# Kernel tuning notes

Measured on AMD Instinct MI355X. Metric: run time of the kernel, lower is better.

## Reference

```python
import jax, jax.numpy as jnp
import numpy as np
import math

B, N, D, H = 4, 2048, 1024, 16
DH = D // H  # dim per head
OUT = 1024

def setup_inputs() -> dict:
    key0 = jax.random.key(0)
    ks = jax.random.split(key0, 12)
    s = 1.0 / math.sqrt(D)
    return {
        "key": jax.random.normal(ks[0], (B, N, D), jnp.float32),
        "value": jax.random.normal(ks[1], (B, N, D), jnp.float32),
        "query": jax.random.normal(ks[2], (B, N, D), jnp.float32),
        "Wk": jax.random.normal(ks[3], (D, D), jnp.float32) * s,
        "bk": jax.random.normal(ks[4], (D,), jnp.float32) * 0.01,
        "Wv": jax.random.normal(ks[5], (D, D), jnp.float32) * s,
        "bv": jax.random.normal(ks[6], (D,), jnp.float32) * 0.01,
        "Wq": jax.random.normal(ks[7], (D, D), jnp.float32) * s,
        "bq": jax.random.normal(ks[8], (D,), jnp.float32) * 0.01,
        "Wo": jax.random.normal(ks[9], (D, OUT), jnp.float32) * s,
        "bo": jax.random.normal(ks[10], (OUT,), jnp.float32) * 0.01,
    }

def reference(key, value, query, Wk, bk, Wv, bv, Wq, bq, Wo, bo):
    scale = math.sqrt(DH)
    k = (key @ Wk + bk).reshape(B, N, H, DH).transpose(0, 2, 1, 3)    # [B,H,N,DH]
    v = (value @ Wv + bv).reshape(B, N, H, DH).transpose(0, 2, 1, 3)
    q = ((query @ Wq + bq) / scale).reshape(B, N, H, DH).transpose(0, 2, 1, 3)
    scores = jnp.einsum('bhqd,bhkd->bhqk', q, k).astype(jnp.float32)  # [B,H,N,N]
    attn = jax.nn.softmax(scores, axis=-1).astype(q.dtype)
    # dropout p=0.0 (eval / identity)
    ctx = jnp.einsum('bhqk,bhkd->bhqd', attn, v)                      # [B,H,N,DH]
    ctx = ctx.transpose(0, 2, 1, 3).reshape(B, N, D)
    out = ctx @ Wo + bo                                               # [B,N,OUT]
    return out
```

## Files before the change

### kernel.cpp

```cpp
#include <hip/hip_runtime.h>
#include <hip/hip_bf16.h>
#include <stdint.h>

#define BB 4
#define NN 2048
#define DD 1024
#define HH 16
#define DHH 64
#define MM (BB*NN)

typedef unsigned short u16;
typedef unsigned int u32;
typedef __bf16 bf16x8_t __attribute__((ext_vector_type(8)));
typedef float f32x4_t __attribute__((ext_vector_type(4)));
typedef float f32x16_t __attribute__((ext_vector_type(16)));

__device__ inline u16 f2b(float f) {
    __hip_bfloat16 h = __float2bfloat16(f);
    return *(u16*)&h;
}

__device__ inline u32 pack2(float lo, float hi) {
    __hip_bfloat162 h2 = __float22bfloat162_rn(make_float2(lo, hi));
    return *(u32*)&h2;
}

__device__ inline void gload16(const void* g, void* l) {
    __builtin_amdgcn_global_load_lds(
        (const __attribute__((address_space(1))) void*)g,
        (__attribute__((address_space(3))) void*)l, 16, 0, 0);
}

__global__ void cvt_kernel(const float* __restrict__ in, u16* __restrict__ out) {
    int i = (blockIdx.x * 256 + threadIdx.x) * 4;
    float4 v = *(const float4*)(in + i);
    ushort4 o;
    o.x = f2b(v.x); o.y = f2b(v.y); o.z = f2b(v.z); o.w = f2b(v.w);
    *(ushort4*)(out + i) = o;
}

__global__ void wtrans_kernel(const float* __restrict__ W0, const float* __restrict__ W1,
                              const float* __restrict__ W2, const float* __restrict__ W3,
                              u16* __restrict__ out_base) {
    int z = blockIdx.z;
    const float* W = (z == 0) ? W0 : (z == 1) ? W1 : (z == 2) ? W2 : W3;
    u16* o = out_base + (size_t)z * DD * DD;
    __shared__ float tile[64][65];
    int t = threadIdx.x;
    int r0 = t >> 6;
    int c = t & 63;
    int kb = blockIdx.x, nb = blockIdx.y;
#pragma unroll
    for (int i = 0; i < 16; ++i) {
        int r = i * 4 + r0;
        tile[r][c] = W[(size_t)(kb * 64 + r) * DD + nb * 64 + c];
    }
    __syncthreads();
#pragma unroll
    for (int i = 0; i < 16; ++i) {
        int r = i * 4 + r0;
        o[(size_t)(nb * 64 + r) * DD + kb * 64 + c] = f2b(tile[c][r]);
    }
}

__global__ void vtrans_kernel(const u16* __restrict__ in, u16* __restrict__ out) {
    __shared__ u16 tile[64][65];
    const int t = threadIdx.x;
    const int r0 = t >> 6;
    const int c = t & 63;
    const int nt = blockIdx.x;
    const int bh = blockIdx.y;
    const int b = bh >> 4, h = bh & 15;
    const u16* src = in + ((size_t)(b * 2048 + nt * 64)) * DD + h * 64;
#pragma unroll
    for (int i = 0; i < 16; ++i) {
        int r = i * 4 + r0;
        tile[r][c] = src[(size_t)r * DD + c];
    }
    __syncthreads();
    u16* dst = out + ((size_t)bh * 64) * NN + nt * 64;
#pragma unroll
    for (int i = 0; i < 16; ++i) {
        int r = i * 4 + r0;
        dst[(size_t)r * NN + c] = tile[c][r];
    }
}

template<int OUT_F32>
__global__ __launch_bounds__(256, 2)
void gemm_bt(const u16* __restrict__ A, const u16* __restrict__ Bt,
             const float* __restrict__ bias, void* __restrict__ Cout, float scale) {
    __shared__ u16 As[128 * 64];
    __shared__ u16 Bs[128 * 64];
    const int t = threadIdx.x;
    const int w = t >> 6, l = t & 63;
    const int wm = w >> 1, wn = w & 1;
    const int g = l >> 4, c = l & 15;
    const int bm = blockIdx.x, bn = blockIdx.y;

    const f32x4_t vzero = {0.f, 0.f, 0.f, 0.f};
    f32x4_t acc[4][4];
#pragma unroll
    for (int m = 0; m < 4; ++m)
#pragma unroll
        for (int n = 0; n < 4; ++n) acc[m][n] = vzero;

    const int srow = l >> 3;
    const int scol = ((l & 7) ^ srow) << 3;
    const int sa = (l & 7) << 4;

    for (int ks = 0; ks < 16; ++ks) {
#pragma unroll
        for (int i = 0; i < 4; ++i) {
            int chunk = w * 4 + i;
            int row = chunk * 8 + srow;
            const u16* ga = A + (size_t)(bm * 128 + row) * DD + ks * 64 + scol;
            gload16(ga, As + chunk * 512);
            const u16* gb = Bt + (size_t)(bn * 128 + row) * DD + ks * 64 + scol;
            gload16(gb, Bs + chunk * 512);
        }
        __syncthreads();

        bf16x8_t af[4][2], bfr[4][2];
#pragma unroll
        for (int m = 0; m < 4; ++m) {
            int rowa = wm * 64 + m * 16 + c;
#pragma unroll
            for (int kk = 0; kk < 2; ++kk)
                af[m][kk] = *(const bf16x8_t*)&As[rowa * 64 + (((kk * 64 + g * 16) ^ sa) >> 1)];
        }
#pragma unroll
        for (int n = 0; n < 4; ++n) {
            int rowb = wn * 64 + n * 16 + c;
#pragma unroll
            for (int kk = 0; kk < 2; ++kk)
                bfr[n][kk] = *(const bf16x8_t*)&Bs[rowb * 64 + (((kk * 64 + g * 16) ^ sa) >> 1)];
        }
#pragma unroll
        for (int kk = 0; kk < 2; ++kk)
#pragma unroll
            for (int m = 0; m < 4; ++m)
#pragma unroll
                for (int n = 0; n < 4; ++n)
                    acc[m][n] = __builtin_amdgcn_mfma_f32_16x16x32_bf16(
                        af[m][kk], bfr[n][kk], acc[m][n], 0, 0, 0);
        __syncthreads();
    }

#pragma unroll
    for (int n = 0; n < 4; ++n) {
        int col = bn * 128 + wn * 64 + n * 16 + c;
        float bv = bias[col];
#pragma unroll
        for (int m = 0; m < 4; ++m) {
            int row = bm * 128 + wm * 64 + m * 16 + g * 4;
#pragma unroll
            for (int j = 0; j < 4; ++j) {
                float v = (acc[m][n][j] + bv) * scale;
                if (OUT_F32)
                    ((float*)Cout)[(size_t)(row + j) * DD + col] = v;
                else
                    ((u16*)Cout)[(size_t)(row + j) * DD + col] = f2b(v);
            }
        }
    }
}

__global__ __launch_bounds__(256, 2)
void attn32_kernel(const u16* __restrict__ qb, const u16* __restrict__ kb,
                   const u16* __restrict__ vt, u16* __restrict__ ctx) {
    __shared__ u16 Kt[2][64 * 64];
    __shared__ u16 Vs[2][64 * 64];
    const int t = threadIdx.x;
    const int w = t >> 6, l = t & 63;
    const int hl = l >> 5, l31 = l & 31, l7 = l & 7, l3 = l >> 3;

    const int f = blockIdx.y * 8 + blockIdx.x;
    const int wg = (f & 7) * 64 + (f >> 3);
    const int qt = wg & 7, bh = wg >> 3;
    const int b = bh >> 4, h = bh & 15;
    const int hoff = h * DHH;
    const size_t kv0 = (size_t)b * NN;
    const size_t vt0 = (size_t)bh * DHH;

    const size_t qrow_base = (size_t)(b * NN + qt * 256 + w * 64);
    bf16x8_t qf[2][4];
#pragma unroll
    for (int qm = 0; qm < 2; ++qm)
#pragma unroll
        for (int dks = 0; dks < 4; ++dks)
            qf[qm][dks] = *(const bf16x8_t*)&qb[(qrow_base + qm * 32 + l31) * DD +
                                                hoff + dks * 16 + hl * 8];

    f32x16_t accO[2][2];
#pragma unroll
    for (int qm = 0; qm < 2; ++qm)
#pragma unroll
        for (int dt = 0; dt < 2; ++dt)
#pragma unroll
            for (int r = 0; r < 16; ++r) accO[qm][dt][r] = 0.f;
    float lacc[2] = {0.f, 0.f};

    const int scol2 = (l7 ^ l3) << 3;
    const u16* kp[2];
    const u16* vp[2];
#pragma unroll
    for (int i = 0; i < 2; ++i) {
        const int ch = w * 2 + i, r = ch * 8 + l3, rr = (r >> 2) & 3;
        const int pr = (rr == 1 || rr == 2) ? (r ^ 12) : r;
        kp[i] = kb + (kv0 + pr) * DD + hoff + scol2;
        vp[i] = vt + (vt0 + r) * NN + scol2;
    }

#define STAGE(buf_)                                                          \
    do {                                                                     \
        _Pragma("unroll")                                                    \
        for (int i_ = 0; i_ < 2; ++i_) {                                     \
            gload16(kp[i_], &Kt[buf_][(w * 2 + i_) * 512]);                  \
            gload16(vp[i_], &Vs[buf_][(w * 2 + i_) * 512]);                  \
        }                                                                    \
        _Pragma("unroll")                                                    \
        for (int i_ = 0; i_ < 2; ++i_) { kp[i_] += 64 * DD; vp[i_] += 64; }  \
    } while (0)

    STAGE(0);

    for (int kt = 0; kt < NN / 64; ++kt) {
        const int cur = kt & 1;
        if (kt < NN / 64 - 1) {
            STAGE(cur ^ 1);
            asm volatile("s_waitcnt vmcnt(4)" ::: "memory");
        } else {
            asm volatile("s_waitcnt vmcnt(0)" ::: "memory");
        }
        __builtin_amdgcn_s_barrier();
        asm volatile("" ::: "memory");

        const char* Kc = (const char*)Kt[cur];
        const char* Vc = (const char*)Vs[cur];

        bf16x8_t kf[2][4];
#pragma unroll
        for (int kt32 = 0; kt32 < 2; ++kt32)
#pragma unroll
            for (int dks = 0; dks < 4; ++dks)
                kf[kt32][dks] = *(const bf16x8_t*)(Kc + (kt32 * 32 + l31) * 128 +
                                                   ((dks * 32 + hl * 16) ^ (l7 << 4)));

        f32x16_t accS[2][2];
        __builtin_amdgcn_s_setprio(1);
#pragma unroll
        for (int qm = 0; qm < 2; ++qm)
#pragma unroll
            for (int kt32 = 0; kt32 < 2; ++kt32) {
#pragma unroll
                for (int r = 0; r < 16; ++r) accS[qm][kt32][r] = 0.f;
#pragma unroll
                for (int dks = 0; dks < 4; ++dks)
                    accS[qm][kt32] = __builtin_amdgcn_mfma_f32_32x32x16_bf16(
                        kf[kt32][dks], qf[qm][dks], accS[qm][kt32], 0, 0, 0);
            }
        __builtin_amdgcn_s_setprio(0);

#pragma unroll
        for (int qm = 0; qm < 2; ++qm) {
#pragma unroll
            for (int kt32 = 0; kt32 < 2; ++kt32)
#pragma unroll
                for (int r = 0; r < 16; ++r)
                    accS[qm][kt32][r] = __builtin_amdgcn_exp2f(accS[qm][kt32][r]);
            f32x16_t sv = accS[qm][0] + accS[qm][1];
            float s8[8];
#pragma unroll
            for (int r = 0; r < 8; ++r) s8[r] = sv[r] + sv[r + 8];
#pragma unroll
            for (int sl = 4; sl >= 1; sl >>= 1)
#pragma unroll
                for (int r = 0; r < sl; ++r) s8[r] += s8[r + sl];
            lacc[qm] += s8[0];
        }

        bf16x8_t vf[4][2];
#pragma unroll
        for (int pm = 0; pm < 4; ++pm)
#pragma unroll
            for (int dt = 0; dt < 2; ++dt)
                vf[pm][dt] = *(const bf16x8_t*)(Vc + (dt * 32 + l31) * 128 +
                                                ((pm * 32 + hl * 16) ^ (l7 << 4)));

        __builtin_amdgcn_s_setprio(1);
#pragma unroll
        for (int qm = 0; qm < 2; ++qm)
#pragma unroll
            for (int pm = 0; pm < 4; ++pm) {
                const int kt32 = pm >> 1, half = pm & 1;
                union { u32 u[4]; bf16x8_t v; } pu;
#pragma unroll
                for (int j2 = 0; j2 < 4; ++j2)
                    pu.u[j2] = pack2(accS[qm][kt32][half * 8 + 2 * j2],
                                     accS[qm][kt32][half * 8 + 2 * j2 + 1]);
#pragma unroll
                for (int dt = 0; dt < 2; ++dt)
                    accO[qm][dt] = __builtin_amdgcn_mfma_f32_32x32x16_bf16(
                        vf[pm][dt], pu.v, accO[qm][dt], 0, 0, 0);
            }
        __builtin_amdgcn_s_setprio(0);

        asm volatile("" ::: "memory");
        __builtin_amdgcn_s_barrier();
        asm volatile("" ::: "memory");
    }
#undef STAGE

#pragma unroll
    for (int qm = 0; qm < 2; ++qm) {
        float rsum = lacc[qm] + __shfl_xor(lacc[qm], 32);
        const float rl = 1.0f / rsum;
        const size_t qrow = qrow_base + qm * 32 + l31;
#pragma unroll
        for (int dt = 0; dt < 2; ++dt)
#pragma unroll
            for (int m = 0; m < 4; ++m) {
                ushort4 o;
                o.x = f2b(accO[qm][dt][4 * m + 0] * rl);
                o.y = f2b(accO[qm][dt][4 * m + 1] * rl);
                o.z = f2b(accO[qm][dt][4 * m + 2] * rl);
                o.w = f2b(accO[qm][dt][4 * m + 3] * rl);
                *(ushort4*)&ctx[qrow * DD + hoff + dt * 32 + m * 8 + hl * 4] = o;
            }
    }
}

extern "C" void kernel_launch(void* const* d_in, const int* in_sizes, int n_in,
                              void* d_out, int out_size, void* d_ws, size_t ws_size,
                              hipStream_t stream) {
    (void)in_sizes; (void)n_in; (void)out_size; (void)ws_size;
    const float* key   = (const float*)d_in[0];
    const float* value = (const float*)d_in[1];
    const float* query = (const float*)d_in[2];
    const float* Wk = (const float*)d_in[3];
    const float* bk = (const float*)d_in[4];
    const float* Wv = (const float*)d_in[5];
    const float* bv = (const float*)d_in[6];
    const float* Wq = (const float*)d_in[7];
    const float* bq = (const float*)d_in[8];
    const float* Wo = (const float*)d_in[9];
    const float* bo = (const float*)d_in[10];

    char* ws = (char*)d_ws;
    const size_t MB = 1024 * 1024;
    u16* qbuf = (u16*)(ws + 0 * MB);
    u16* kbuf = (u16*)(ws + 16 * MB);
    u16* vbuf = (u16*)(ws + 32 * MB);
    u16* WtK  = (u16*)(ws + 48 * MB);
    u16* WtV  = (u16*)(ws + 50 * MB);
    u16* WtQ  = (u16*)(ws + 52 * MB);
    u16* WtO  = (u16*)(ws + 54 * MB);
    u16* xb   = (u16*)(ws + 56 * MB);

    const int nelem = MM * DD;
    const int cvt_blocks = nelem / (256 * 4);

    wtrans_kernel<<<dim3(16, 16, 4), 256, 0, stream>>>(Wk, Wv, Wq, Wo, WtK);

    cvt_kernel<<<cvt_blocks, 256, 0, stream>>>(value, xb);
    gemm_bt<0><<<dim3(64, 8), 256, 0, stream>>>(xb, WtV, bv, vbuf, 1.0f);
    cvt_kernel<<<cvt_blocks, 256, 0, stream>>>(key, xb);
    gemm_bt<0><<<dim3(64, 8), 256, 0, stream>>>(xb, WtK, bk, kbuf, 1.0f);
    cvt_kernel<<<cvt_blocks, 256, 0, stream>>>(query, xb);
    gemm_bt<0><<<dim3(64, 8), 256, 0, stream>>>(xb, WtQ, bq, qbuf, 0.125f * 1.4426950408889634f);

    u16* VT = xb;
    vtrans_kernel<<<dim3(32, 64), 256, 0, stream>>>(vbuf, VT);

    u16* ctx = vbuf;
    attn32_kernel<<<dim3(8, 64), 256, 0, stream>>>(qbuf, kbuf, VT, ctx);

    gemm_bt<1><<<dim3(64, 8), 256, 0, stream>>>(ctx, WtO, bo, d_out, 1.0f);
}
```

Baseline: 211.0 us.

## Process two KV tiles per barrier with quad-buffered LDS in attention

The attention loop now stages two 64-row K/V tiles at a time into a four-slot LDS ring and computes both before the next barrier. This halves the number of barriers and waitcnts per KV token and lets the loop use precomputed, statically offset LDS addresses instead of per-iteration buffer selection. The first MFMA of each score tile now takes a zero vector as its accumulator instead of a separately zeroed one. LDS use doubles to 64 KB per block, which may limit how many blocks fit per CU alongside the launch bound of 2.

```diff
diff --git a/kernel.cpp b/kernel.cpp
--- a/kernel.cpp
+++ b/kernel.cpp
@@ -169,8 +169,8 @@
 __global__ __launch_bounds__(256, 2)
 void attn32_kernel(const u16* __restrict__ qb, const u16* __restrict__ kb,
                    const u16* __restrict__ vt, u16* __restrict__ ctx) {
-    __shared__ u16 Kt[2][64 * 64];
-    __shared__ u16 Vs[2][64 * 64];
+    __shared__ u16 KL[4][64 * 64];
+    __shared__ u16 VL[4][64 * 64];
     const int t = threadIdx.x;
     const int w = t >> 6, l = t & 63;
     const int hl = l >> 5, l31 = l & 31, l7 = l & 7, l3 = l >> 3;
@@ -192,14 +192,24 @@
             qf[qm][dks] = *(const bf16x8_t*)&qb[(qrow_base + qm * 32 + l31) * DD +
                                                 hoff + dks * 16 + hl * 8];
 
+    f32x16_t z16;
+#pragma unroll
+    for (int r = 0; r < 16; ++r) z16[r] = 0.f;
+
     f32x16_t accO[2][2];
 #pragma unroll
     for (int qm = 0; qm < 2; ++qm)
 #pragma unroll
-        for (int dt = 0; dt < 2; ++dt)
-#pragma unroll
-            for (int r = 0; r < 16; ++r) accO[qm][dt][r] = 0.f;
+        for (int dt = 0; dt < 2; ++dt) accO[qm][dt] = z16;
     float lacc[2] = {0.f, 0.f};
+
+    const char* kAd[4];
+    const char* vAd[4];
+#pragma unroll
+    for (int d = 0; d < 4; ++d) {
+        kAd[d] = (const char*)KL + l31 * 128 + ((d * 32 + hl * 16) ^ (l7 << 4));
+        vAd[d] = (const char*)VL + l31 * 128 + ((d * 32 + hl * 16) ^ (l7 << 4));
+    }
 
     const int scol2 = (l7 ^ l3) << 3;
     const u16* kp[2];
@@ -212,105 +222,113 @@
         vp[i] = vt + (vt0 + r) * NN + scol2;
     }
 
-#define STAGE(buf_)                                                          \
+#define STAGE1(S_)                                                           \
     do {                                                                     \
         _Pragma("unroll")                                                    \
         for (int i_ = 0; i_ < 2; ++i_) {                                     \
-            gload16(kp[i_], &Kt[buf_][(w * 2 + i_) * 512]);                  \
-            gload16(vp[i_], &Vs[buf_][(w * 2 + i_) * 512]);                  \
+            gload16(kp[i_], &KL[S_][(w * 2 + i_) * 512]);                    \
+            gload16(vp[i_], &VL[S_][(w * 2 + i_) * 512]);                    \
         }                                                                    \
         _Pragma("unroll")                                                    \
         for (int i_ = 0; i_ < 2; ++i_) { kp[i_] += 64 * DD; vp[i_] += 64; }  \
     } while (0)
 
-    STAGE(0);
-
-    for (int kt = 0; kt < NN / 64; ++kt) {
-        const int cur = kt & 1;
-        if (kt < NN / 64 - 1) {
-            STAGE(cur ^ 1);
-            asm volatile("s_waitcnt vmcnt(4)" ::: "memory");
-        } else {
-            asm volatile("s_waitcnt vmcnt(0)" ::: "memory");
-        }
-        __builtin_amdgcn_s_barrier();
-        asm volatile("" ::: "memory");
-
-        const char* Kc = (const char*)Kt[cur];
-        const char* Vc = (const char*)Vs[cur];
-
-        bf16x8_t kf[2][4];
-#pragma unroll
-        for (int kt32 = 0; kt32 < 2; ++kt32)
-#pragma unroll
-            for (int dks = 0; dks < 4; ++dks)
-                kf[kt32][dks] = *(const bf16x8_t*)(Kc + (kt32 * 32 + l31) * 128 +
-                                                   ((dks * 32 + hl * 16) ^ (l7 << 4)));
-
-        f32x16_t accS[2][2];
-        __builtin_amdgcn_s_setprio(1);
-#pragma unroll
-        for (int qm = 0; qm < 2; ++qm)
-#pragma unroll
-            for (int kt32 = 0; kt32 < 2; ++kt32) {
-#pragma unroll
-                for (int r = 0; r < 16; ++r) accS[qm][kt32][r] = 0.f;
-#pragma unroll
-                for (int dks = 0; dks < 4; ++dks)
-                    accS[qm][kt32] = __builtin_amdgcn_mfma_f32_32x32x16_bf16(
-                        kf[kt32][dks], qf[qm][dks], accS[qm][kt32], 0, 0, 0);
-            }
-        __builtin_amdgcn_s_setprio(0);
-
-#pragma unroll
-        for (int qm = 0; qm < 2; ++qm) {
-#pragma unroll
-            for (int kt32 = 0; kt32 < 2; ++kt32)
-#pragma unroll
-                for (int r = 0; r < 16; ++r)
-                    accS[qm][kt32][r] = __builtin_amdgcn_exp2f(accS[qm][kt32][r]);
-            f32x16_t sv = accS[qm][0] + accS[qm][1];
-            float s8[8];
-#pragma unroll
-            for (int r = 0; r < 8; ++r) s8[r] = sv[r] + sv[r + 8];
-#pragma unroll
-            for (int sl = 4; sl >= 1; sl >>= 1)
-#pragma unroll
-                for (int r = 0; r < sl; ++r) s8[r] += s8[r + sl];
-            lacc[qm] += s8[0];
-        }
-
-        bf16x8_t vf[4][2];
-#pragma unroll
-        for (int pm = 0; pm < 4; ++pm)
-#pragma unroll
-            for (int dt = 0; dt < 2; ++dt)
-                vf[pm][dt] = *(const bf16x8_t*)(Vc + (dt * 32 + l31) * 128 +
-                                                ((pm * 32 + hl * 16) ^ (l7 << 4)));
-
-        __builtin_amdgcn_s_setprio(1);
-#pragma unroll
-        for (int qm = 0; qm < 2; ++qm)
-#pragma unroll
-            for (int pm = 0; pm < 4; ++pm) {
-                const int kt32 = pm >> 1, half = pm & 1;
-                union { u32 u[4]; bf16x8_t v; } pu;
-#pragma unroll
-                for (int j2 = 0; j2 < 4; ++j2)
-                    pu.u[j2] = pack2(accS[qm][kt32][half * 8 + 2 * j2],
-                                     accS[qm][kt32][half * 8 + 2 * j2 + 1]);
-#pragma unroll
-                for (int dt = 0; dt < 2; ++dt)
-                    accO[qm][dt] = __builtin_amdgcn_mfma_f32_32x32x16_bf16(
-                        vf[pm][dt], pu.v, accO[qm][dt], 0, 0, 0);
-            }
-        __builtin_amdgcn_s_setprio(0);
-
-        asm volatile("" ::: "memory");
-        __builtin_amdgcn_s_barrier();
-        asm volatile("" ::: "memory");
-    }
-#undef STAGE
+#define COMPUTE(S_)                                                          \
+    do {                                                                     \
+        bf16x8_t kf[2][4];                                                   \
+        _Pragma("unroll")                                                    \
+        for (int kt32 = 0; kt32 < 2; ++kt32)                                 \
+            _Pragma("unroll")                                                \
+            for (int dks = 0; dks < 4; ++dks)                                \
+                kf[kt32][dks] = *(const bf16x8_t*)(kAd[dks] + (S_) * 8192 +  \
+                                                   kt32 * 4096);             \
+        f32x16_t accS[2][2];                                                 \
+        __builtin_amdgcn_s_setprio(1);                                       \
+        _Pragma("unroll")                                                    \
+        for (int qm = 0; qm < 2; ++qm)                                       \
+            _Pragma("unroll")                                                \
+            for (int kt32 = 0; kt32 < 2; ++kt32) {                           \
+                accS[qm][kt32] = __builtin_amdgcn_mfma_f32_32x32x16_bf16(    \
+                    kf[kt32][0], qf[qm][0], z16, 0, 0, 0);                   \
+                _Pragma("unroll")                                            \
+                for (int dks = 1; dks < 4; ++dks)                            \
+                    accS[qm][kt32] = __builtin_amdgcn_mfma_f32_32x32x16_bf16(\
+                        kf[kt32][dks], qf[qm][dks], accS[qm][kt32], 0, 0, 0);\
+            }                                                                \
+        __builtin_amdgcn_s_setprio(0);                                       \
+        _Pragma("unroll")                                                    \
+        for (int qm = 0; qm < 2; ++qm) {                                     \
+            _Pragma("unroll")                                                \
+            for (int kt32 = 0; kt32 < 2; ++kt32)                             \
+                _Pragma("unroll")                                            \
+                for (int r = 0; r < 16; ++r)                                 \
+                    accS[qm][kt32][r] =                                      \
+                        __builtin_amdgcn_exp2f(accS[qm][kt32][r]);           \
+            f32x16_t sv = accS[qm][0] + accS[qm][1];                         \
+            float s8[8];                                                     \
+            _Pragma("unroll")                                                \
+            for (int r = 0; r < 8; ++r) s8[r] = sv[r] + sv[r + 8];           \
+            _Pragma("unroll")                                                \
+            for (int sl = 4; sl >= 1; sl >>= 1)                              \
+                _Pragma("unroll")                                            \
+                for (int r = 0; r < sl; ++r) s8[r] += s8[r + sl];            \
+            lacc[qm] += s8[0];                                               \
+        }                                                                    \
+        bf16x8_t vf[4][2];                                                   \
+        _Pragma("unroll")                                                    \
+        for (int pm = 0; pm < 4; ++pm)                                       \
+            _Pragma("unroll")                                                \
+            for (int dt = 0; dt < 2; ++dt)                                   \
+                vf[pm][dt] = *(const bf16x8_t*)(vAd[pm] + (S_) * 8192 +      \
+                                                dt * 4096);                  \
+        __builtin_amdgcn_s_setprio(1);                                       \
+        _Pragma("unroll")                                                    \
+        for (int qm = 0; qm < 2; ++qm)                                       \
+            _Pragma("unroll")                                                \
+            for (int pm = 0; pm < 4; ++pm) {                                 \
+                const int kt32_ = pm >> 1, half_ = pm & 1;                   \
+                union { u32 u[4]; bf16x8_t v; } pu;                          \
+                _Pragma("unroll")                                            \
+                for (int j2 = 0; j2 < 4; ++j2)                               \
+                    pu.u[j2] = pack2(accS[qm][kt32_][half_ * 8 + 2 * j2],    \
+                                     accS[qm][kt32_][half_ * 8 + 2 * j2 + 1]); \
+                _Pragma("unroll")                                            \
+                for (int dt = 0; dt < 2; ++dt)                               \
+                    accO[qm][dt] = __builtin_amdgcn_mfma_f32_32x32x16_bf16(  \
+                        vf[pm][dt], pu.v, accO[qm][dt], 0, 0, 0);            \
+            }                                                                \
+        __builtin_amdgcn_s_setprio(0);                                       \
+    } while (0)
+
+#define PAIRSTEP(CS_, OS_, LAST_)                                            \
+    do {                                                                     \
+        if (!(LAST_)) {                                                      \
+            STAGE1(OS_);                                                     \
+            STAGE1((OS_) + 1);                                               \
+            asm volatile("s_waitcnt vmcnt(8)" ::: "memory");                 \
+        } else {                                                             \
+            asm volatile("s_waitcnt vmcnt(0)" ::: "memory");                 \
+        }                                                                    \
+        __builtin_amdgcn_s_barrier();                                        \
+        asm volatile("" ::: "memory");                                       \
+        COMPUTE(CS_);                                                        \
+        COMPUTE((CS_) + 1);                                                  \
+        asm volatile("" ::: "memory");                                       \
+        __builtin_amdgcn_s_barrier();                                        \
+        asm volatile("" ::: "memory");                                       \
+    } while (0)
+
+    STAGE1(0);
+    STAGE1(1);
+
+#pragma unroll 1
+    for (int pp = 0; pp < 8; ++pp) {
+        PAIRSTEP(0, 2, 0);
+        PAIRSTEP(2, 0, pp == 7);
+    }
+#undef STAGE1
+#undef COMPUTE
+#undef PAIRSTEP
 
 #pragma unroll
     for (int qm = 0; qm < 2; ++qm) {
```

After: 219.4 us. 4.0% more time.

## Deepen K/V prefetch to four-stage ring and defer row-sum reduction

Applied to the files above, without the earlier changes.

Changes the attention kernel's K/V LDS staging from double buffering to a four-slot ring with three tiles in flight, adjusting the vmcnt waits for the tail iterations. Row-sum accumulation now keeps a 16-wide vector accumulator per query tile and does the horizontal reduction once at the end instead of every tile. The first MFMA also takes a zero vector directly rather than zero-initialising accumulators. The aim is to hide global load latency and cut per-iteration VALU work, at the cost of doubled LDS (64KB per block) and more registers, which may reduce occupancy below the requested two blocks.

```diff
diff --git a/kernel.cpp b/kernel.cpp
--- a/kernel.cpp
+++ b/kernel.cpp
@@ -169,8 +169,8 @@
 __global__ __launch_bounds__(256, 2)
 void attn32_kernel(const u16* __restrict__ qb, const u16* __restrict__ kb,
                    const u16* __restrict__ vt, u16* __restrict__ ctx) {
-    __shared__ u16 Kt[2][64 * 64];
-    __shared__ u16 Vs[2][64 * 64];
+    __shared__ u16 Kt[4][64 * 64];
+    __shared__ u16 Vs[4][64 * 64];
     const int t = threadIdx.x;
     const int w = t >> 6, l = t & 63;
     const int hl = l >> 5, l31 = l & 31, l7 = l & 7, l3 = l >> 3;
@@ -192,14 +192,17 @@
             qf[qm][dks] = *(const bf16x8_t*)&qb[(qrow_base + qm * 32 + l31) * DD +
                                                 hoff + dks * 16 + hl * 8];
 
+    f32x16_t z16;
+#pragma unroll
+    for (int r = 0; r < 16; ++r) z16[r] = 0.f;
+
     f32x16_t accO[2][2];
 #pragma unroll
     for (int qm = 0; qm < 2; ++qm)
 #pragma unroll
-        for (int dt = 0; dt < 2; ++dt)
-#pragma unroll
-            for (int r = 0; r < 16; ++r) accO[qm][dt][r] = 0.f;
-    float lacc[2] = {0.f, 0.f};
+        for (int dt = 0; dt < 2; ++dt) accO[qm][dt] = z16;
+    f32x16_t lacc16[2];
+    lacc16[0] = z16; lacc16[1] = z16;
 
     const int scol2 = (l7 ^ l3) << 3;
     const u16* kp[2];
@@ -212,23 +215,30 @@
         vp[i] = vt + (vt0 + r) * NN + scol2;
     }
 
-#define STAGE(buf_)                                                          \
+#define STAGE(S_)                                                            \
     do {                                                                     \
         _Pragma("unroll")                                                    \
         for (int i_ = 0; i_ < 2; ++i_) {                                     \
-            gload16(kp[i_], &Kt[buf_][(w * 2 + i_) * 512]);                  \
-            gload16(vp[i_], &Vs[buf_][(w * 2 + i_) * 512]);                  \
+            gload16(kp[i_], &Kt[S_][(w * 2 + i_) * 512]);                    \
+            gload16(vp[i_], &Vs[S_][(w * 2 + i_) * 512]);                    \
         }                                                                    \
         _Pragma("unroll")                                                    \
         for (int i_ = 0; i_ < 2; ++i_) { kp[i_] += 64 * DD; vp[i_] += 64; }  \
     } while (0)
 
     STAGE(0);
-
+    STAGE(1);
+    STAGE(2);
+
+#pragma unroll 1
     for (int kt = 0; kt < NN / 64; ++kt) {
-        const int cur = kt & 1;
-        if (kt < NN / 64 - 1) {
-            STAGE(cur ^ 1);
+        const int cur = kt & 3;
+        if (kt < NN / 64 - 3) {
+            STAGE((kt + 3) & 3);
+            asm volatile("s_waitcnt vmcnt(12)" ::: "memory");
+        } else if (kt == NN / 64 - 3) {
+            asm volatile("s_waitcnt vmcnt(8)" ::: "memory");
+        } else if (kt == NN / 64 - 2) {
             asm volatile("s_waitcnt vmcnt(4)" ::: "memory");
         } else {
             asm volatile("s_waitcnt vmcnt(0)" ::: "memory");
@@ -253,10 +263,10 @@
         for (int qm = 0; qm < 2; ++qm)
 #pragma unroll
             for (int kt32 = 0; kt32 < 2; ++kt32) {
-#pragma unroll
-                for (int r = 0; r < 16; ++r) accS[qm][kt32][r] = 0.f;
-#pragma unroll
-                for (int dks = 0; dks < 4; ++dks)
+                accS[qm][kt32] = __builtin_amdgcn_mfma_f32_32x32x16_bf16(
+                    kf[kt32][0], qf[qm][0], z16, 0, 0, 0);
+#pragma unroll
+                for (int dks = 1; dks < 4; ++dks)
                     accS[qm][kt32] = __builtin_amdgcn_mfma_f32_32x32x16_bf16(
                         kf[kt32][dks], qf[qm][dks], accS[qm][kt32], 0, 0, 0);
             }
@@ -269,15 +279,7 @@
 #pragma unroll
                 for (int r = 0; r < 16; ++r)
                     accS[qm][kt32][r] = __builtin_amdgcn_exp2f(accS[qm][kt32][r]);
-            f32x16_t sv = accS[qm][0] + accS[qm][1];
-            float s8[8];
-#pragma unroll
-            for (int r = 0; r < 8; ++r) s8[r] = sv[r] + sv[r + 8];
-#pragma unroll
-            for (int sl = 4; sl >= 1; sl >>= 1)
-#pragma unroll
-                for (int r = 0; r < sl; ++r) s8[r] += s8[r + sl];
-            lacc[qm] += s8[0];
+            lacc16[qm] += accS[qm][0] + accS[qm][1];
         }
 
         bf16x8_t vf[4][2];
@@ -314,7 +316,14 @@
 
 #pragma unroll
     for (int qm = 0; qm < 2; ++qm) {
-        float rsum = lacc[qm] + __shfl_xor(lacc[qm], 32);
+        float s8[8];
+#pragma unroll
+        for (int r = 0; r < 8; ++r) s8[r] = lacc16[qm][r] + lacc16[qm][r + 8];
+#pragma unroll
+        for (int sl = 4; sl >= 1; sl >>= 1)
+#pragma unroll
+            for (int r = 0; r < sl; ++r) s8[r] += s8[r + sl];
+        float rsum = s8[0] + __shfl_xor(s8[0], 32);
         const float rl = 1.0f / rsum;
         const size_t qrow = qrow_base + qm * 32 + l31;
 #pragma unroll
```

After: 208.9 us. About the same (-1.0%).

## Halve attention query tile per wave to raise occupancy and grid size

Applied to the files above, without the earlier changes.

Each wave in the attention kernel now handles 32 query rows instead of 64, so a block covers 128 rows and the grid doubles to 1024 blocks. Launch bounds rise to 4 blocks per CU, with fewer accumulator registers and a deferred row-sum reduction (8 partials kept and reduced once at the end). This is meant to improve latency hiding and CU fill, but each K/V tile loaded into LDS is now reused by half as many queries, doubling K/V global traffic.

```diff
diff --git a/kernel.cpp b/kernel.cpp
--- a/kernel.cpp
+++ b/kernel.cpp
@@ -166,7 +166,7 @@
     }
 }
 
-__global__ __launch_bounds__(256, 2)
+__global__ __launch_bounds__(256, 4)
 void attn32_kernel(const u16* __restrict__ qb, const u16* __restrict__ kb,
                    const u16* __restrict__ vt, u16* __restrict__ ctx) {
     __shared__ u16 Kt[2][64 * 64];
@@ -175,31 +175,28 @@
     const int w = t >> 6, l = t & 63;
     const int hl = l >> 5, l31 = l & 31, l7 = l & 7, l3 = l >> 3;
 
-    const int f = blockIdx.y * 8 + blockIdx.x;
-    const int wg = (f & 7) * 64 + (f >> 3);
-    const int qt = wg & 7, bh = wg >> 3;
+    const int f = blockIdx.y * 16 + blockIdx.x;
+    const int wg = (f & 7) * 128 + (f >> 3);
+    const int qt = wg & 15, bh = wg >> 4;
     const int b = bh >> 4, h = bh & 15;
     const int hoff = h * DHH;
     const size_t kv0 = (size_t)b * NN;
     const size_t vt0 = (size_t)bh * DHH;
 
-    const size_t qrow_base = (size_t)(b * NN + qt * 256 + w * 64);
-    bf16x8_t qf[2][4];
-#pragma unroll
-    for (int qm = 0; qm < 2; ++qm)
-#pragma unroll
-        for (int dks = 0; dks < 4; ++dks)
-            qf[qm][dks] = *(const bf16x8_t*)&qb[(qrow_base + qm * 32 + l31) * DD +
-                                                hoff + dks * 16 + hl * 8];
-
-    f32x16_t accO[2][2];
-#pragma unroll
-    for (int qm = 0; qm < 2; ++qm)
-#pragma unroll
-        for (int dt = 0; dt < 2; ++dt)
-#pragma unroll
-            for (int r = 0; r < 16; ++r) accO[qm][dt][r] = 0.f;
-    float lacc[2] = {0.f, 0.f};
+    const size_t qrow = (size_t)(b * NN + qt * 128 + w * 32 + l31);
+    bf16x8_t qf[4];
+#pragma unroll
+    for (int dks = 0; dks < 4; ++dks)
+        qf[dks] = *(const bf16x8_t*)&qb[qrow * DD + hoff + dks * 16 + hl * 8];
+
+    f32x16_t accO[2];
+#pragma unroll
+    for (int dt = 0; dt < 2; ++dt)
+#pragma unroll
+        for (int r = 0; r < 16; ++r) accO[dt][r] = 0.f;
+    float lacc8[8];
+#pragma unroll
+    for (int r = 0; r < 8; ++r) lacc8[r] = 0.f;
 
     const int scol2 = (l7 ^ l3) << 3;
     const u16* kp[2];
@@ -225,6 +222,7 @@
 
     STAGE(0);
 
+#pragma unroll 1
     for (int kt = 0; kt < NN / 64; ++kt) {
         const int cur = kt & 1;
         if (kt < NN / 64 - 1) {
@@ -247,38 +245,27 @@
                 kf[kt32][dks] = *(const bf16x8_t*)(Kc + (kt32 * 32 + l31) * 128 +
                                                    ((dks * 32 + hl * 16) ^ (l7 << 4)));
 
-        f32x16_t accS[2][2];
+        f32x16_t accS[2];
         __builtin_amdgcn_s_setprio(1);
 #pragma unroll
-        for (int qm = 0; qm < 2; ++qm)
-#pragma unroll
-            for (int kt32 = 0; kt32 < 2; ++kt32) {
-#pragma unroll
-                for (int r = 0; r < 16; ++r) accS[qm][kt32][r] = 0.f;
-#pragma unroll
-                for (int dks = 0; dks < 4; ++dks)
-                    accS[qm][kt32] = __builtin_amdgcn_mfma_f32_32x32x16_bf16(
-                        kf[kt32][dks], qf[qm][dks], accS[qm][kt32], 0, 0, 0);
-            }
+        for (int kt32 = 0; kt32 < 2; ++kt32) {
+#pragma unroll
+            for (int r = 0; r < 16; ++r) accS[kt32][r] = 0.f;
+#pragma unroll
+            for (int dks = 0; dks < 4; ++dks)
+                accS[kt32] = __builtin_amdgcn_mfma_f32_32x32x16_bf16(
+                    kf[kt32][dks], qf[dks], accS[kt32], 0, 0, 0);
+        }
         __builtin_amdgcn_s_setprio(0);
 
 #pragma unroll
-        for (int qm = 0; qm < 2; ++qm) {
-#pragma unroll
-            for (int kt32 = 0; kt32 < 2; ++kt32)
-#pragma unroll
-                for (int r = 0; r < 16; ++r)
-                    accS[qm][kt32][r] = __builtin_amdgcn_exp2f(accS[qm][kt32][r]);
-            f32x16_t sv = accS[qm][0] + accS[qm][1];
-            float s8[8];
-#pragma unroll
-            for (int r = 0; r < 8; ++r) s8[r] = sv[r] + sv[r + 8];
-#pragma unroll
-            for (int sl = 4; sl >= 1; sl >>= 1)
-#pragma unroll
-                for (int r = 0; r < sl; ++r) s8[r] += s8[r + sl];
-            lacc[qm] += s8[0];
-        }
+        for (int kt32 = 0; kt32 < 2; ++kt32)
+#pragma unroll
+            for (int r = 0; r < 16; ++r)
+                accS[kt32][r] = __builtin_amdgcn_exp2f(accS[kt32][r]);
+#pragma unroll
+        for (int r = 0; r < 8; ++r)
+            lacc8[r] += (accS[0][r] + accS[0][r + 8]) + (accS[1][r] + accS[1][r + 8]);
 
         bf16x8_t vf[4][2];
 #pragma unroll
@@ -290,20 +277,18 @@
 
         __builtin_amdgcn_s_setprio(1);
 #pragma unroll
-        for (int qm = 0; qm < 2; ++qm)
-#pragma unroll
-            for (int pm = 0; pm < 4; ++pm) {
-                const int kt32 = pm >> 1, half = pm & 1;
-                union { u32 u[4]; bf16x8_t v; } pu;
-#pragma unroll
-                for (int j2 = 0; j2 < 4; ++j2)
-                    pu.u[j2] = pack2(accS[qm][kt32][half * 8 + 2 * j2],
-                                     accS[qm][kt32][half * 8 + 2 * j2 + 1]);
-#pragma unroll
-                for (int dt = 0; dt < 2; ++dt)
-                    accO[qm][dt] = __builtin_amdgcn_mfma_f32_32x32x16_bf16(
-                        vf[pm][dt], pu.v, accO[qm][dt], 0, 0, 0);
-            }
+        for (int pm = 0; pm < 4; ++pm) {
+            const int kt32 = pm >> 1, half = pm & 1;
+            union { u32 u[4]; bf16x8_t v; } pu;
+#pragma unroll
+            for (int j2 = 0; j2 < 4; ++j2)
+                pu.u[j2] = pack2(accS[kt32][half * 8 + 2 * j2],
+                                 accS[kt32][half * 8 + 2 * j2 + 1]);
+#pragma unroll
+            for (int dt = 0; dt < 2; ++dt)
+                accO[dt] = __builtin_amdgcn_mfma_f32_32x32x16_bf16(
+                    vf[pm][dt], pu.v, accO[dt], 0, 0, 0);
+        }
         __builtin_amdgcn_s_setprio(0);
 
         asm volatile("" ::: "memory");
@@ -312,23 +297,26 @@
     }
 #undef STAGE
 
-#pragma unroll
-    for (int qm = 0; qm < 2; ++qm) {
-        float rsum = lacc[qm] + __shfl_xor(lacc[qm], 32);
-        const float rl = 1.0f / rsum;
-        const size_t qrow = qrow_base + qm * 32 + l31;
-#pragma unroll
-        for (int dt = 0; dt < 2; ++dt)
-#pragma unroll
-            for (int m = 0; m < 4; ++m) {
-                ushort4 o;
-                o.x = f2b(accO[qm][dt][4 * m + 0] * rl);
-                o.y = f2b(accO[qm][dt][4 * m + 1] * rl);
-                o.z = f2b(accO[qm][dt][4 * m + 2] * rl);
-                o.w = f2b(accO[qm][dt][4 * m + 3] * rl);
-                *(ushort4*)&ctx[qrow * DD + hoff + dt * 32 + m * 8 + hl * 4] = o;
-            }
-    }
+    float s8[8];
+#pragma unroll
+    for (int r = 0; r < 8; ++r) s8[r] = lacc8[r];
+#pragma unroll
+    for (int sl = 4; sl >= 1; sl >>= 1)
+#pragma unroll
+        for (int r = 0; r < sl; ++r) s8[r] += s8[r + sl];
+    float rsum = s8[0] + __shfl_xor(s8[0], 32);
+    const float rl = 1.0f / rsum;
+#pragma unroll
+    for (int dt = 0; dt < 2; ++dt)
+#pragma unroll
+        for (int m = 0; m < 4; ++m) {
+            ushort4 o;
+            o.x = f2b(accO[dt][4 * m + 0] * rl);
+            o.y = f2b(accO[dt][4 * m + 1] * rl);
+            o.z = f2b(accO[dt][4 * m + 2] * rl);
+            o.w = f2b(accO[dt][4 * m + 3] * rl);
+            *(ushort4*)&ctx[qrow * DD + hoff + dt * 32 + m * 8 + hl * 4] = o;
+        }
 }
 
 extern "C" void kernel_launch(void* const* d_in, const int* in_sizes, int n_in,
@@ -374,7 +362,7 @@
     vtrans_kernel<<<dim3(32, 64), 256, 0, stream>>>(vbuf, VT);
 
     u16* ctx = vbuf;
-    attn32_kernel<<<dim3(8, 64), 256, 0, stream>>>(qbuf, kbuf, VT, ctx);
+    attn32_kernel<<<dim3(16, 64), 256, 0, stream>>>(qbuf, kbuf, VT, ctx);
 
     gemm_bt<1><<<dim3(64, 8), 256, 0, stream>>>(ctx, WtO, bo, d_out, 1.0f);
 }
```

Result: slower. 221.8 us (+5.1%).
